# Optimization experiments

Measured on AMD Instinct MI355X. Metric: run time of the kernel, lower is better.

The kernel has to match this reference:

```python
import jax, jax.numpy as jnp
import numpy as np

D_MODEL = 1024
N_SH = 16            # sub-heads per branch
N_BR = 4             # branches
H_TOT = N_BR * N_SH  # 64 total heads
DH = D_MODEL // N_SH # 64 head dim
BRANCH_CONFIGS = [(16, 0), (128, 16), (128, 0), (512, 144)]


def rms_norm(x):
    eps = jnp.finfo(x.dtype).eps
    return x * jax.lax.rsqrt(jnp.mean(x * x, axis=-1, keepdims=True) + eps)


def rope(x):
    # x: [B, H, T, Dh]; non-standard RoPE: even/odd split, halves concatenated
    T, Dh = x.shape[2], x.shape[3]
    inv_freq = 1.0 / (10000.0 ** (jnp.arange(0, Dh, 2, dtype=jnp.float32) / Dh))
    freqs = jnp.arange(T, dtype=jnp.float32)[:, None] * inv_freq[None, :]  # [T, Dh/2]
    cos = jnp.cos(freqs)[None, None]
    sin = jnp.sin(freqs)[None, None]
    x1 = x[..., 0::2]
    x2 = x[..., 1::2]
    return jnp.concatenate([-x2 * sin + x1 * cos, x1 * sin + x2 * cos], axis=-1)


def setup_inputs() -> dict:
    key = jax.random.key(0)
    ks = jax.random.split(key, 12)
    B, T, C = 2, 1024, D_MODEL
    s = 0.02
    return {
        "X": jax.random.normal(ks[0], (B, T, C), jnp.float32),
        "WQ": jax.random.normal(ks[1], (C, H_TOT * DH), jnp.float32) * s,
        "bQ": jax.random.normal(ks[2], (H_TOT * DH,), jnp.float32) * s,
        "WK": jax.random.normal(ks[3], (C, C), jnp.float32) * s,
        "bK": jax.random.normal(ks[4], (C,), jnp.float32) * s,
        "WV": jax.random.normal(ks[5], (C, H_TOT * DH), jnp.float32) * s,
        "bV": jax.random.normal(ks[6], (H_TOT * DH,), jnp.float32) * s,
        "WO": jax.random.normal(ks[7], (C, C), jnp.float32) * s,
        "bO": jax.random.normal(ks[8], (C,), jnp.float32) * s,
        "sink_scalars": jax.random.normal(ks[9], (H_TOT,), jnp.float32) * s,
        "v_nulls": jax.random.normal(ks[10], (H_TOT, DH), jnp.float32) * s,
    }


def reference(X, WQ, bQ, WK, bK, WV, bV, WO, bO, sink_scalars, v_nulls):
    B, T, C = X.shape
    # projections -> [B, H, T, Dh]
    q = (X @ WQ + bQ).reshape(B, T, H_TOT, DH).transpose(0, 2, 1, 3)
    q = rope(rms_norm(q))
    v = (X @ WV + bV).reshape(B, T, H_TOT, DH).transpose(0, 2, 1, 3)
    k = rope((X @ WK + bK).reshape(B, T, N_SH, DH).transpose(0, 2, 1, 3))
    k = jnp.tile(k, (1, N_BR, 1, 1))  # [B, H_TOT, T, Dh]

    # KMax scores with key self-norm denominator
    scores = jnp.einsum('bhqd,bhkd->bhqk', q, k)
    denom = jnp.sqrt(jnp.sum(k * k, axis=-1))[:, :, None, :]  # [B,H,1,T]
    w = scores / denom

    # banded masks per branch; note: off-band logits become 0 (NOT -inf) -> exp(0)=1 in softmax
    idx = jnp.arange(T)
    dist = idx[:, None] - idx[None, :]  # query - key
    bmasks = jnp.stack([((dist >= g) & (dist < h)).astype(w.dtype)
                        for (h, g) in BRANCH_CONFIGS], axis=0)  # [N_BR,T,T]
    full_mask = jnp.repeat(bmasks, N_SH, axis=0)[None]  # [1,H_TOT,T,T] (band subset of tril)
    w = w * full_mask

    # learnable tanh sink logit per head, concatenated as extra column
    sinks = jnp.broadcast_to(jnp.tanh(sink_scalars).reshape(1, H_TOT, 1, 1), (B, H_TOT, T, 1))
    probs = jax.nn.softmax(jnp.concatenate([w, sinks], axis=-1), axis=-1)

    out = jnp.einsum('bhqk,bhkd->bhqd', probs[..., :T], v)
    out = out + probs[..., T:] * v_nulls.reshape(1, H_TOT, 1, DH)

    # [B,H_TOT,T,Dh] -> [B,N_BR,T,C]
    ctx = out.reshape(B, N_BR, N_SH, T, DH).transpose(0, 1, 3, 2, 4).reshape(B, N_BR, T, C)
    y = ctx @ WO + bO
    return y.mean(axis=1)
```

## Files before the change

kernel.cpp:

```cpp
#include <hip/hip_runtime.h>
#include <hip/hip_bf16.h>
#include <math.h>

#define T_SEQ 1024
#define LOG2_10000 13.287712379549449f

typedef unsigned short u16;
typedef unsigned int u32;
typedef __attribute__((ext_vector_type(8))) short bf16x8;
typedef __attribute__((ext_vector_type(4))) float f32x4;

__device__ __forceinline__ void gload16(const u16* g, const u16* s) {
  __builtin_amdgcn_global_load_lds(
      (const __attribute__((address_space(1))) void*)g,
      (__attribute__((address_space(3))) void*)s, 16, 0, 0);
}

__device__ __forceinline__ u16 f2bf(float x) {
  __hip_bfloat16 h = __float2bfloat16(x);
  return *reinterpret_cast<u16*>(&h);
}
__device__ __forceinline__ float bf2f(u16 x) {
  __hip_bfloat16 h = *reinterpret_cast<__hip_bfloat16*>(&x);
  return __bfloat162float(h);
}

__device__ __forceinline__ void transpose_step(
    const float* __restrict__ W, u16* __restrict__ Wt, int N, int nbx,
    int local, int t, float (*tile)[33]) {
  int bx = local % nbx, by = local / nbx;
  int n0 = bx * 32, k0 = by * 32;
  int r = t >> 3, c4 = (t & 7) * 4;
  float4 v = *reinterpret_cast<const float4*>(&W[(size_t)(k0 + r) * N + n0 + c4]);
  tile[r][c4 + 0] = v.x;
  tile[r][c4 + 1] = v.y;
  tile[r][c4 + 2] = v.z;
  tile[r][c4 + 3] = v.w;
  __syncthreads();
  u16 o[4];
#pragma unroll
  for (int i = 0; i < 4; ++i) o[i] = f2bf(tile[c4 + i][r]);
  *reinterpret_cast<uint2*>(&Wt[(size_t)(n0 + r) * 1024 + k0 + c4]) =
      *reinterpret_cast<const uint2*>(o);
}

__global__ __launch_bounds__(256) void prep_kernel(
    const float* __restrict__ X, const float* __restrict__ WQ,
    const float* __restrict__ WK, const float* __restrict__ WV,
    const float* __restrict__ WO, const float* __restrict__ bQ,
    const float* __restrict__ bV, const float* __restrict__ bK,
    u16* __restrict__ Xb, u16* __restrict__ WQVKt, u16* __restrict__ WOt,
    float* __restrict__ bQVK, float* __restrict__ ctab, float* __restrict__ stab)
{
  __shared__ float tile[32][33];
  const int blk = blockIdx.x, t = threadIdx.x;
  if (blk < 128) {
    int id = blk * 256 + t;
    int tt = id >> 5, p = id & 31;
    float invf = exp2f(-LOG2_10000 * (float)(2 * p) * (1.0f / 64.0f));
    float ang = (float)tt * invf;
    float sn, cs;
    sincosf(ang, &sn, &cs);
    ctab[id] = cs;
    stab[id] = sn;
  } else if (blk < 1152) {
    int i = (blk - 128) * 256 + t;
    float4 a = reinterpret_cast<const float4*>(X)[2 * i];
    float4 b = reinterpret_cast<const float4*>(X)[2 * i + 1];
    u16 o[8] = {f2bf(a.x), f2bf(a.y), f2bf(a.z), f2bf(a.w),
                f2bf(b.x), f2bf(b.y), f2bf(b.z), f2bf(b.w)};
    reinterpret_cast<uint4*>(Xb)[i] = *reinterpret_cast<const uint4*>(o);
  } else if (blk < 5248) {
    transpose_step(WQ, WQVKt, 4096, 128, blk - 1152, t, tile);
  } else if (blk < 9344) {
    transpose_step(WV, WQVKt + (size_t)4096 * 1024, 4096, 128, blk - 5248, t, tile);
  } else if (blk < 10368) {
    transpose_step(WK, WQVKt + (size_t)8192 * 1024, 1024, 32, blk - 9344, t, tile);
  } else if (blk < 11392) {
    transpose_step(WO, WOt, 1024, 32, blk - 10368, t, tile);
  } else {
    int id = (blk - 11392) * 256 + t;
    if (id < 9216)
      bQVK[id] = (id < 4096) ? bQ[id] : (id < 8192) ? bV[id - 4096] : bK[id - 8192];
  }
}

__global__ __launch_bounds__(256) void xsum_part_kernel(
    const float* __restrict__ X, float* __restrict__ part) {
  int blk = blockIdx.x;
  int b = blk >> 6, tc = blk & 63;
  const float* base = X + (size_t)(b * 1024 + tc * 16) * 1024;
  for (int kk = threadIdx.x; kk < 1024; kk += 256) {
    float s = 0.f;
#pragma unroll
    for (int tt = 0; tt < 16; ++tt) s += base[(size_t)tt * 1024 + kk];
    part[(size_t)blk * 1024 + kk] = s;
  }
}

__global__ __launch_bounds__(256) void xsum_reduce_kernel(
    const float* __restrict__ part, float* __restrict__ Xsum) {
  int id = blockIdx.x * 256 + threadIdx.x;
  int b = id >> 10, k = id & 1023;
  float s = 0.f;
#pragma unroll 8
  for (int i = 0; i < 64; ++i) s += part[(size_t)(b * 64 + i) * 1024 + k];
  Xsum[id] = s;
}

__global__ __launch_bounds__(256) void vgemv_part_kernel(
    const float* __restrict__ Xsum, const float* __restrict__ WV,
    float* __restrict__ part2) {
  __shared__ float xs0[128], xs1[128];
  int blk = blockIdx.x;
  int nc = blk & 15, ks = blk >> 4;
  int n = nc * 256 + threadIdx.x;
  int k0 = ks * 128;
  if (threadIdx.x < 128) xs0[threadIdx.x] = Xsum[k0 + threadIdx.x];
  else xs1[threadIdx.x - 128] = Xsum[1024 + k0 + threadIdx.x - 128];
  __syncthreads();
  float a0 = 0.f, a1 = 0.f;
  for (int k = 0; k < 128; ++k) {
    float w = WV[(size_t)(k0 + k) * 4096 + n];
    a0 = fmaf(xs0[k], w, a0);
    a1 = fmaf(xs1[k], w, a1);
  }
  part2[(size_t)(ks * 2 + 0) * 4096 + n] = a0;
  part2[(size_t)(ks * 2 + 1) * 4096 + n] = a1;
}

__global__ __launch_bounds__(256) void vgemv_reduce_kernel(
    const float* __restrict__ part2, const float* __restrict__ bV,
    float* __restrict__ Vsum) {
  int id = blockIdx.x * 256 + threadIdx.x;
  int b = id >> 12, n = id & 4095;
  float s = 1024.0f * bV[n];
#pragma unroll
  for (int ks = 0; ks < 8; ++ks) s += part2[(size_t)(ks * 2 + b) * 4096 + n];
  Vsum[id] = s;
}

__global__ __launch_bounds__(512, 1) void gemm8ph_kernel(
    const u16* __restrict__ Ab, const u16* __restrict__ Bt,
    const float* __restrict__ bias, u16* __restrict__ Cqv)
{
  __shared__ __align__(16) u16 sAb[2][256 * 64];
  __shared__ __align__(16) u16 sBb[2][256 * 64];

  const int tid = threadIdx.x;
  const int lane = tid & 63;
  const int w = tid >> 6;
  const int wm = w >> 2, wn = w & 3;
  const int l15 = lane & 15, l4 = lane >> 4;

  int lin = blockIdx.y * 32 + blockIdx.x;
  lin = (lin & 7) * 32 + (lin >> 3);
  const int bx = lin & 31, by = lin >> 5;
  const int m0 = by * 256, bn0 = bx * 256;

  const int srow = tid >> 3;
  const int csw = (tid & 7) ^ (srow & 7);
  const u16* a_base = Ab + (size_t)(m0 + srow) * 1024 + 8 * csw;
  const u16* b_base = Bt + (size_t)(bn0 + srow) * 1024 + 8 * csw;

  const int ch0 = (0 + l4) ^ (l15 & 7);
  const int ch1 = (4 + l4) ^ (l15 & 7);

  f32x4 acc[8][4];
#pragma unroll
  for (int i = 0; i < 8; ++i)
#pragma unroll
    for (int j = 0; j < 4; ++j) acc[i][j] = (f32x4){0.f, 0.f, 0.f, 0.f};

#define STAGE8(kt, buf)                                                        \
  {                                                                            \
    const u16* ga = a_base + (kt) * 64;                                        \
    const u16* gb = b_base + (kt) * 64;                                        \
    u16* da = &sAb[buf][tid * 8];                                              \
    u16* db = &sBb[buf][tid * 8];                                              \
    _Pragma("unroll") for (int q = 0; q < 4; ++q) {                            \
      gload16(ga + q * 65536, da + q * 4096);                                  \
      gload16(gb + q * 65536, db + q * 4096);                                  \
    }                                                                          \
  }

  STAGE8(0, 0);
#pragma unroll 1
  for (int kt = 0; kt < 16; ++kt) {
    const int buf = kt & 1;
    if (kt < 15) {
      STAGE8(kt + 1, buf ^ 1);
      asm volatile("s_waitcnt vmcnt(8)" ::: "memory");
    } else {
      asm volatile("s_waitcnt vmcnt(0)" ::: "memory");
    }
    __builtin_amdgcn_sched_barrier(0);
    __builtin_amdgcn_s_barrier();
    __builtin_amdgcn_sched_barrier(0);

    const u16* tA = sAb[buf];
    const u16* tB = sBb[buf];

    bf16x8 bfv[4][2];
#pragma unroll
    for (int n = 0; n < 4; ++n) {
      int row = wn * 64 + n * 16 + l15;
      bfv[n][0] = *reinterpret_cast<const bf16x8*>(&tB[row * 64 + ch0 * 8]);
      bfv[n][1] = *reinterpret_cast<const bf16x8*>(&tB[row * 64 + ch1 * 8]);
    }
#pragma unroll
    for (int mh = 0; mh < 2; ++mh) {
      bf16x8 af[4][2];
#pragma unroll
      for (int m = 0; m < 4; ++m) {
        int row = wm * 128 + mh * 64 + m * 16 + l15;
        af[m][0] = *reinterpret_cast<const bf16x8*>(&tA[row * 64 + ch0 * 8]);
        af[m][1] = *reinterpret_cast<const bf16x8*>(&tA[row * 64 + ch1 * 8]);
      }
      __builtin_amdgcn_s_setprio(1);
#pragma unroll
      for (int kk = 0; kk < 2; ++kk)
#pragma unroll
        for (int m = 0; m < 4; ++m)
#pragma unroll
          for (int n = 0; n < 4; ++n)
            acc[mh * 4 + m][n] = __builtin_amdgcn_mfma_f32_16x16x32_bf16(
                af[m][kk], bfv[n][kk], acc[mh * 4 + m][n], 0, 0, 0);
      __builtin_amdgcn_s_setprio(0);
    }
    __builtin_amdgcn_s_barrier();
    __builtin_amdgcn_sched_barrier(0);
  }
#undef STAGE8

#pragma unroll
  for (int n = 0; n < 4; ++n) {
    int col = bn0 + wn * 64 + n * 16 + l15;
    float bv = bias[col];
#pragma unroll
    for (int mf = 0; mf < 8; ++mf) {
#pragma unroll
      for (int r = 0; r < 4; ++r) {
        int row = m0 + wm * 128 + mf * 16 + l4 * 4 + r;
        Cqv[(size_t)row * 8192 + col] = f2bf(acc[mf][n][r] + bv);
      }
    }
  }
}

template <bool BF16OUT>
__global__ __launch_bounds__(256) void gemm64_kernel(
    const u16* __restrict__ Ab, const u16* __restrict__ Bt,
    const float* __restrict__ bias, void* __restrict__ Cv,
    int M, int N, int K)
{
  __shared__ __align__(16) u16 sA[64 * 32];
  __shared__ __align__(16) u16 sB[64 * 32];
  const int tid = threadIdx.x;
  const int lane = tid & 63;
  const int wv = tid >> 6;
  const int wm = wv >> 1, wn = wv & 1;
  const int l15 = lane & 15, l4 = lane >> 4;
  const int m0 = blockIdx.y * 64, n0 = blockIdx.x * 64;

  f32x4 acc[2][2];
#pragma unroll
  for (int i = 0; i < 2; ++i)
#pragma unroll
    for (int j = 0; j < 2; ++j) acc[i][j] = (f32x4){0.f, 0.f, 0.f, 0.f};

  const int r0 = tid >> 2, kc = tid & 3;
  const u16* a_src = Ab + (size_t)(m0 + r0) * K + kc * 8;
  const u16* b_src = Bt + (size_t)(n0 + r0) * K + kc * 8;
  u16* dA = sA + (size_t)wv * 512;
  u16* dB = sB + (size_t)wv * 512;
  const int kcol = l4 * 8;

  for (int k0 = 0; k0 < K; k0 += 32) {
    __syncthreads();
    gload16(a_src + k0, dA);
    gload16(b_src + k0, dB);
    __syncthreads();
    bf16x8 af[2], bfv[2];
#pragma unroll
    for (int mi = 0; mi < 2; ++mi)
      af[mi] = *reinterpret_cast<const bf16x8*>(&sA[(wm * 32 + mi * 16 + l15) * 32 + kcol]);
#pragma unroll
    for (int ni = 0; ni < 2; ++ni)
      bfv[ni] = *reinterpret_cast<const bf16x8*>(&sB[(wn * 32 + ni * 16 + l15) * 32 + kcol]);
#pragma unroll
    for (int mi = 0; mi < 2; ++mi)
#pragma unroll
      for (int ni = 0; ni < 2; ++ni)
        acc[mi][ni] = __builtin_amdgcn_mfma_f32_16x16x32_bf16(
            af[mi], bfv[ni], acc[mi][ni], 0, 0, 0);
  }

#pragma unroll
  for (int mi = 0; mi < 2; ++mi)
#pragma unroll
    for (int ni = 0; ni < 2; ++ni) {
      int col = n0 + wn * 32 + ni * 16 + l15;
      float bv = bias[col];
#pragma unroll
      for (int r = 0; r < 4; ++r) {
        int row = m0 + wm * 32 + mi * 16 + l4 * 4 + r;
        float val = acc[mi][ni][r] + bv;
        size_t idx = (size_t)row * N + col;
        if (BF16OUT) ((u16*)Cv)[idx] = f2bf(val);
        else ((float*)Cv)[idx] = val;
      }
    }
}

__global__ __launch_bounds__(256) void qk_transform_kernel(
    u16* __restrict__ QVbf, u16* __restrict__ Kbf,
    const float* __restrict__ ctab, const float* __restrict__ stab)
{
  const int rid  = blockIdx.x * 8 + (threadIdx.x >> 5);
  const int lane = threadIdx.x & 63;
  const int p    = lane & 31;
  const int gb   = lane & 32;

  u16* row;
  int t;
  const bool isQ = rid < 131072;
  if (isQ) {
    int h = rid & 63, bt = rid >> 6;
    t = bt & 1023;
    row = QVbf + (size_t)bt * 8192 + h * 64;
  } else {
    int r2 = rid - 131072;
    int hsL = r2 & 15, bt = r2 >> 4;
    t = bt & 1023;
    row = Kbf + (size_t)bt * 1024 + hsL * 64;
  }

  u32 v = reinterpret_cast<const u32*>(row)[p];
  float x1 = bf2f((u16)v), x2 = bf2f((u16)(v >> 16));
  float cs = ctab[t * 32 + p], sn = stab[t * 32 + p];

  float o_lo, o_hi;
  if (isQ) {
    float ss = x1 * x1 + x2 * x2;
    ss += __shfl_xor(ss, 1, 64);
    ss += __shfl_xor(ss, 2, 64);
    ss += __shfl_xor(ss, 4, 64);
    ss += __shfl_xor(ss, 8, 64);
    ss += __shfl_xor(ss, 16, 64);
    float rs = rsqrtf(ss * (1.0f / 64.0f) + 1.1920929e-7f);
    float xn1 = x1 * rs, xn2 = x2 * rs;
    o_lo = xn1 * cs - xn2 * sn;
    o_hi = xn1 * sn + xn2 * cs;
  } else {
    float xr1 = x1 * cs - x2 * sn;
    float xr2 = x1 * sn + x2 * cs;
    float ss = xr1 * xr1 + xr2 * xr2;
    ss += __shfl_xor(ss, 1, 64);
    ss += __shfl_xor(ss, 2, 64);
    ss += __shfl_xor(ss, 4, 64);
    ss += __shfl_xor(ss, 8, 64);
    ss += __shfl_xor(ss, 16, 64);
    float rs = rsqrtf(ss);
    o_lo = xr1 * rs;
    o_hi = xr2 * rs;
  }

  int m = (2 * p) & 31;
  float slo0 = __shfl(o_lo, gb + m, 64);
  float slo1 = __shfl(o_lo, gb + m + 1, 64);
  float shi0 = __shfl(o_hi, gb + m, 64);
  float shi1 = __shfl(o_hi, gb + m + 1, 64);
  float e0 = (p < 16) ? slo0 : shi0;
  float e1 = (p < 16) ? slo1 : shi1;
  reinterpret_cast<u32*>(row)[p] = (u32)f2bf(e0) | ((u32)f2bf(e1) << 16);
}

__global__ __launch_bounds__(256) void attn_mfma_kernel(
    const u16* __restrict__ Qv, const u16* __restrict__ Kb,
    const float* __restrict__ Vsum, const float* __restrict__ sink,
    const float* __restrict__ vnull, u16* __restrict__ mctxb)
{
  __shared__ __align__(16) u16 sQ[64 * 64];
  __shared__ __align__(16) u16 sK[2][64 * 64];
  __shared__ __align__(16) u16 sVt[2][64 * 64];
  __shared__ __align__(16) u16 sP[64 * 64];

  int blk = blockIdx.x;
  blk = (blk & 7) * 64 + (blk >> 3);
  const int qt  = blk & 15;
  const int hs  = (blk >> 4) & 15;
  const int b   = blk >> 8;
  const int qt0 = qt * 64;

  const int tid  = threadIdx.x;
  const int lane = tid & 63;
  const int wv   = tid >> 6;
  const int l15  = lane & 15;
  const int l4   = lane >> 4;
  const int qr0  = tid >> 3, qi0 = tid & 7;
  const int qr1  = qr0 + 32;
  const int vjp  = tid & 31, vdg = tid >> 5;
  const int qrow = wv * 16 + l15;

  constexpr int HCFG[4] = {16, 128, 128, 512};
  constexpr int GCFG[4] = {0, 16, 0, 144};

  f32x4 macc[4];
#pragma unroll
  for (int i = 0; i < 4; ++i) macc[i] = (f32x4){0.f, 0.f, 0.f, 0.f};

#pragma unroll 1
  for (int br = 0; br < 4; ++br) {
    const int h = br * 16 + hs;
    const int hmax = HCFG[br], g = GCFG[br];
    int klo = qt0 - (hmax - 1); if (klo < 0) klo = 0;
    int khi = qt0 + 63 - g;     if (khi > 1023) khi = 1023;
    const int nc = (khi >= klo) ? ((khi - klo) / 64 + 1) : 0;

    gload16(Qv + (size_t)(b * 1024 + qt0 + qr0) * 8192 + h * 64 + 8 * (qi0 ^ (qr0 & 7)),
            sQ + (size_t)wv * 512);
    gload16(Qv + (size_t)(b * 1024 + qt0 + qr1) * 8192 + h * 64 + 8 * (qi0 ^ (qr1 & 7)),
            sQ + 2048 + (size_t)wv * 512);
    bf16x8 va, vb;
    if (nc > 0) {
      int ja0 = klo + qr0; if (ja0 > 1023) ja0 = 1023;
      int ja1 = klo + qr1; if (ja1 > 1023) ja1 = 1023;
      gload16(Kb + (size_t)(b * 1024 + ja0) * 1024 + hs * 64 + 8 * (qi0 ^ (qr0 & 7)),
              sK[0] + (size_t)wv * 512);
      gload16(Kb + (size_t)(b * 1024 + ja1) * 1024 + hs * 64 + 8 * (qi0 ^ (qr1 & 7)),
              sK[0] + 2048 + (size_t)wv * 512);
      int jva = klo + 2 * vjp, jvb = jva + 1;
      if (jva > 1023) jva = 1023;
      if (jvb > 1023) jvb = 1023;
      va = *reinterpret_cast<const bf16x8*>(
          &Qv[(size_t)(b * 1024 + jva) * 8192 + 4096 + h * 64 + vdg * 8]);
      vb = *reinterpret_cast<const bf16x8*>(
          &Qv[(size_t)(b * 1024 + jvb) * 8192 + 4096 + h * 64 + vdg * 8]);
    }
    asm volatile("s_waitcnt vmcnt(0)" ::: "memory");
    __builtin_amdgcn_sched_barrier(0);
    if (nc > 0) {
#pragma unroll
      for (int e = 0; e < 8; ++e) {
        int d = vdg * 8 + e;
        u32 pack = (u32)(u16)va[e] | ((u32)(u16)vb[e] << 16);
        *reinterpret_cast<u32*>(
            (char*)sVt[0] + d * 128 + ((4 * vjp) ^ ((d & 7) << 4))) = pack;
      }
    }
    asm volatile("s_waitcnt lgkmcnt(0)" ::: "memory");
    __builtin_amdgcn_sched_barrier(0);
    __builtin_amdgcn_s_barrier();

    bf16x8 afQ[2];
#pragma unroll
    for (int kh = 0; kh < 2; ++kh) {
      int cs = (4 * kh + l4) ^ (l15 & 7);
      afQ[kh] = *reinterpret_cast<const bf16x8*>(&sQ[qrow * 64 + cs * 8]);
    }

    f32x4 outv[4];
#pragma unroll
    for (int i = 0; i < 4; ++i) outv[i] = (f32x4){0.f, 0.f, 0.f, 0.f};
    float zacc[4] = {0.f, 0.f, 0.f, 0.f};

    int buf = 0;
#pragma unroll 1
    for (int c = 0; c < nc; ++c) {
      const int j0 = klo + c * 64;
      const bool nxt = (c + 1 < nc);
      if (nxt) {
        int j0n = j0 + 64;
        int ja0 = j0n + qr0; if (ja0 > 1023) ja0 = 1023;
        int ja1 = j0n + qr1; if (ja1 > 1023) ja1 = 1023;
        gload16(Kb + (size_t)(b * 1024 + ja0) * 1024 + hs * 64 + 8 * (qi0 ^ (qr0 & 7)),
                sK[buf ^ 1] + (size_t)wv * 512);
        gload16(Kb + (size_t)(b * 1024 + ja1) * 1024 + hs * 64 + 8 * (qi0 ^ (qr1 & 7)),
                sK[buf ^ 1] + 2048 + (size_t)wv * 512);
        int jva = j0n + 2 * vjp, jvb = jva + 1;
        if (jva > 1023) jva = 1023;
        if (jvb > 1023) jvb = 1023;
        va = *reinterpret_cast<const bf16x8*>(
            &Qv[(size_t)(b * 1024 + jva) * 8192 + 4096 + h * 64 + vdg * 8]);
        vb = *reinterpret_cast<const bf16x8*>(
            &Qv[(size_t)(b * 1024 + jvb) * 8192 + 4096 + h * 64 + vdg * 8]);
      }
      f32x4 sfr[4];
#pragma unroll
      for (int jt = 0; jt < 4; ++jt) {
        int krow = jt * 16 + l15;
        f32x4 acc = (f32x4){0.f, 0.f, 0.f, 0.f};
#pragma unroll
        for (int kh = 0; kh < 2; ++kh) {
          int cs = (4 * kh + l4) ^ (l15 & 7);
          bf16x8 bk = *reinterpret_cast<const bf16x8*>(&sK[buf][krow * 64 + cs * 8]);
          acc = __builtin_amdgcn_mfma_f32_16x16x32_bf16(afQ[kh], bk, acc, 0, 0, 0);
        }
        sfr[jt] = acc;
      }
#pragma unroll
      for (int jt = 0; jt < 4; ++jt) {
        int jloc = jt * 16 + l15;
        int jabs = j0 + jloc;
#pragma unroll
        for (int r = 0; r < 4; ++r) {
          int q_r = wv * 16 + l4 * 4 + r;
          int dist = (qt0 + q_r) - jabs;
          bool inband = (dist >= g) & (dist < hmax) & (jabs < 1024);
          float pv = inband ? (__expf(sfr[jt][r]) - 1.0f) : 0.0f;
          zacc[r] += pv;
          *reinterpret_cast<u16*>(
              (char*)sP + q_r * 128 + ((2 * jloc) ^ ((q_r & 7) << 4))) = f2bf(pv);
        }
      }
      asm volatile("s_waitcnt lgkmcnt(0)" ::: "memory");
      __builtin_amdgcn_sched_barrier(0);
      bf16x8 afP[2];
#pragma unroll
      for (int kh = 0; kh < 2; ++kh) {
        int cs = (4 * kh + l4) ^ (l15 & 7);
        afP[kh] = *reinterpret_cast<const bf16x8*>(&sP[qrow * 64 + cs * 8]);
      }
#pragma unroll
      for (int dt = 0; dt < 4; ++dt) {
        int drow = dt * 16 + l15;
#pragma unroll
        for (int kh = 0; kh < 2; ++kh) {
          int cs = (4 * kh + l4) ^ (l15 & 7);
          bf16x8 bv = *reinterpret_cast<const bf16x8*>(&sVt[buf][drow * 64 + cs * 8]);
          outv[dt] = __builtin_amdgcn_mfma_f32_16x16x32_bf16(afP[kh], bv, outv[dt], 0, 0, 0);
        }
      }
      if (nxt) {
#pragma unroll
        for (int e = 0; e < 8; ++e) {
          int d = vdg * 8 + e;
          u32 pack = (u32)(u16)va[e] | ((u32)(u16)vb[e] << 16);
          *reinterpret_cast<u32*>(
              (char*)sVt[buf ^ 1] + d * 128 + ((4 * vjp) ^ ((d & 7) << 4))) = pack;
        }
      }
      asm volatile("s_waitcnt vmcnt(0) lgkmcnt(0)" ::: "memory");
      __builtin_amdgcn_sched_barrier(0);
      __builtin_amdgcn_s_barrier();
      buf ^= 1;
    }

#pragma unroll
    for (int r = 0; r < 4; ++r) {
      zacc[r] += __shfl_xor(zacc[r], 1, 64);
      zacc[r] += __shfl_xor(zacc[r], 2, 64);
      zacc[r] += __shfl_xor(zacc[r], 4, 64);
      zacc[r] += __shfl_xor(zacc[r], 8, 64);
    }
    float es = __expf(tanhf(sink[h]));
#pragma unroll
    for (int dt = 0; dt < 4; ++dt) {
      int d = dt * 16 + l15;
      float vs = Vsum[(size_t)b * 4096 + h * 64 + d];
      float vn = vnull[h * 64 + d];
#pragma unroll
      for (int r = 0; r < 4; ++r) {
        float invZ = 1.0f / (1024.0f + zacc[r] + es);
        macc[dt][r] += (outv[dt][r] + vs + es * vn) * invZ;
      }
    }
  }

#pragma unroll
  for (int dt = 0; dt < 4; ++dt) {
#pragma unroll
    for (int r = 0; r < 4; ++r) {
      int q_r = wv * 16 + l4 * 4 + r;
      mctxb[(size_t)(b * 1024 + qt0 + q_r) * 1024 + hs * 64 + dt * 16 + l15] =
          f2bf(0.25f * macc[dt][r]);
    }
  }
}

extern "C" void kernel_launch(void* const* d_in, const int* in_sizes, int n_in,
                              void* d_out, int out_size, void* d_ws, size_t ws_size,
                              hipStream_t stream) {
  (void)in_sizes; (void)n_in; (void)out_size; (void)ws_size;
  const float* X    = (const float*)d_in[0];
  const float* WQ   = (const float*)d_in[1];
  const float* bQ   = (const float*)d_in[2];
  const float* WK   = (const float*)d_in[3];
  const float* bK   = (const float*)d_in[4];
  const float* WV   = (const float*)d_in[5];
  const float* bV   = (const float*)d_in[6];
  const float* WO   = (const float*)d_in[7];
  const float* bO   = (const float*)d_in[8];
  const float* sink = (const float*)d_in[9];
  const float* vnul = (const float*)d_in[10];
  float* Y = (float*)d_out;

  char* p = (char*)d_ws;
  u16*   Xb    = (u16*)p;   p += (size_t)2048 * 1024 * 2;
  u16*   WQVKt = (u16*)p;   p += (size_t)9216 * 1024 * 2;
  u16*   WOt   = (u16*)p;   p += (size_t)1024 * 1024 * 2;
  u16*   QVbf  = (u16*)p;   p += (size_t)2048 * 8192 * 2;
  u16*   Kbf   = (u16*)p;   p += (size_t)2048 * 1024 * 2;
  u16*   mctxb = (u16*)p;   p += (size_t)2048 * 1024 * 2;
  float* Vsum  = (float*)p; p += (size_t)2 * 4096 * 4;
  float* part  = (float*)p; p += (size_t)128 * 1024 * 4;
  float* Xsum  = (float*)p; p += (size_t)2 * 1024 * 4;
  float* part2 = (float*)p; p += (size_t)16 * 4096 * 4;
  float* bQVK  = (float*)p; p += (size_t)9216 * 4;
  float* ctab  = (float*)p; p += (size_t)32768 * 4;
  float* stab  = (float*)p; p += (size_t)32768 * 4;

  dim3 blk(256);
  prep_kernel<<<11428, blk, 0, stream>>>(X, WQ, WK, WV, WO, bQ, bV, bK,
                                         Xb, WQVKt, WOt, bQVK, ctab, stab);
  xsum_part_kernel<<<128, blk, 0, stream>>>(X, part);
  xsum_reduce_kernel<<<8, blk, 0, stream>>>(part, Xsum);
  vgemv_part_kernel<<<128, blk, 0, stream>>>(Xsum, WV, part2);
  vgemv_reduce_kernel<<<32, blk, 0, stream>>>(part2, bV, Vsum);

  gemm8ph_kernel<<<dim3(32, 8), dim3(512), 0, stream>>>(Xb, WQVKt, bQVK, QVbf);
  gemm64_kernel<true><<<dim3(16, 32), blk, 0, stream>>>(
      Xb, WQVKt + (size_t)8192 * 1024, bQVK + 8192, Kbf, 2048, 1024, 1024);

  qk_transform_kernel<<<20480, blk, 0, stream>>>(QVbf, Kbf, ctab, stab);

  attn_mfma_kernel<<<512, blk, 0, stream>>>(QVbf, Kbf, Vsum, sink, vnul, mctxb);

  gemm64_kernel<false><<<dim3(16, 32), blk, 0, stream>>>(mctxb, WOt, bO, Y, 2048, 1024, 1024);
}
```

Baseline: 151.6 us.

## Restructure QV GEMM pipeline and compute V column sums from projected V

The QV projection GEMM switches from a 2-stage pipeline with K-tile 64 to a 4-slot ring with K-tile 32 and prefetch depth 2. It also drops the trailing per-iteration barrier and remaps blocks to XCDs with a new LDS swizzle. The V column-sum path no longer sums X and runs a GEMV with fp32 WV. Instead it sums the bf16 V outputs already produced by the GEMM, which cuts two kernels and the fp32 WV read but adds bf16 rounding to Vsum. Removing the trailing barrier relies on the 4-slot ring to avoid overwriting a buffer that is still being read.

Result: faster. 139.7 us (-7.9%).

```diff
diff --git a/kernel.cpp b/kernel.cpp
--- a/kernel.cpp
+++ b/kernel.cpp
@@ -23,6 +23,16 @@
 __device__ __forceinline__ float bf2f(u16 x) {
   __hip_bfloat16 h = *reinterpret_cast<__hip_bfloat16*>(&x);
   return __bfloat162float(h);
+}
+
+__device__ __forceinline__ float wave_sum64(float v) {
+  v += __shfl_xor(v, 1, 64);
+  v += __shfl_xor(v, 2, 64);
+  v += __shfl_xor(v, 4, 64);
+  v += __shfl_xor(v, 8, 64);
+  v += __shfl_xor(v, 16, 64);
+  v += __shfl_xor(v, 32, 64);
+  return v;
 }
 
 __device__ __forceinline__ void transpose_step(
@@ -85,67 +95,43 @@
   }
 }
 
-__global__ __launch_bounds__(256) void xsum_part_kernel(
-    const float* __restrict__ X, float* __restrict__ part) {
+__global__ __launch_bounds__(256) void vsum_part_kernel(
+    const u16* __restrict__ QVbf, float* __restrict__ part) {
   int blk = blockIdx.x;
-  int b = blk >> 6, tc = blk & 63;
-  const float* base = X + (size_t)(b * 1024 + tc * 16) * 1024;
-  for (int kk = threadIdx.x; kk < 1024; kk += 256) {
-    float s = 0.f;
-#pragma unroll
-    for (int tt = 0; tt < 16; ++tt) s += base[(size_t)tt * 1024 + kk];
-    part[(size_t)blk * 1024 + kk] = s;
-  }
-}
-
-__global__ __launch_bounds__(256) void xsum_reduce_kernel(
-    const float* __restrict__ part, float* __restrict__ Xsum) {
+  int b = blk >> 6, ch = blk & 63;
+  const u16* base = QVbf + (size_t)(b * 1024 + ch * 16) * 8192 + 4096;
+#pragma unroll
+  for (int g = 0; g < 2; ++g) {
+    int c0 = (threadIdx.x + g * 256) * 8;
+    float s[8] = {0.f, 0.f, 0.f, 0.f, 0.f, 0.f, 0.f, 0.f};
+#pragma unroll 4
+    for (int r = 0; r < 16; ++r) {
+      bf16x8 v = *reinterpret_cast<const bf16x8*>(&base[(size_t)r * 8192 + c0]);
+#pragma unroll
+      for (int e = 0; e < 8; ++e) s[e] += bf2f((u16)v[e]);
+    }
+    float* dst = &part[(size_t)blk * 4096 + c0];
+#pragma unroll
+    for (int e = 0; e < 8; ++e) dst[e] = s[e];
+  }
+}
+
+__global__ __launch_bounds__(256) void vsum_reduce_kernel(
+    const float* __restrict__ part, float* __restrict__ Vsum) {
   int id = blockIdx.x * 256 + threadIdx.x;
-  int b = id >> 10, k = id & 1023;
+  int b = id >> 12, n = id & 4095;
   float s = 0.f;
 #pragma unroll 8
-  for (int i = 0; i < 64; ++i) s += part[(size_t)(b * 64 + i) * 1024 + k];
-  Xsum[id] = s;
-}
-
-__global__ __launch_bounds__(256) void vgemv_part_kernel(
-    const float* __restrict__ Xsum, const float* __restrict__ WV,
-    float* __restrict__ part2) {
-  __shared__ float xs0[128], xs1[128];
-  int blk = blockIdx.x;
-  int nc = blk & 15, ks = blk >> 4;
-  int n = nc * 256 + threadIdx.x;
-  int k0 = ks * 128;
-  if (threadIdx.x < 128) xs0[threadIdx.x] = Xsum[k0 + threadIdx.x];
-  else xs1[threadIdx.x - 128] = Xsum[1024 + k0 + threadIdx.x - 128];
-  __syncthreads();
-  float a0 = 0.f, a1 = 0.f;
-  for (int k = 0; k < 128; ++k) {
-    float w = WV[(size_t)(k0 + k) * 4096 + n];
-    a0 = fmaf(xs0[k], w, a0);
-    a1 = fmaf(xs1[k], w, a1);
-  }
-  part2[(size_t)(ks * 2 + 0) * 4096 + n] = a0;
-  part2[(size_t)(ks * 2 + 1) * 4096 + n] = a1;
-}
-
-__global__ __launch_bounds__(256) void vgemv_reduce_kernel(
-    const float* __restrict__ part2, const float* __restrict__ bV,
-    float* __restrict__ Vsum) {
-  int id = blockIdx.x * 256 + threadIdx.x;
-  int b = id >> 12, n = id & 4095;
-  float s = 1024.0f * bV[n];
-#pragma unroll
-  for (int ks = 0; ks < 8; ++ks) s += part2[(size_t)(ks * 2 + b) * 4096 + n];
+  for (int ch = 0; ch < 64; ++ch) s += part[(size_t)(b * 64 + ch) * 4096 + n];
   Vsum[id] = s;
 }
 
-__global__ __launch_bounds__(512, 1) void gemm8ph_kernel(
+__global__ __launch_bounds__(512, 1) void gemm_qv_kernel(
     const u16* __restrict__ Ab, const u16* __restrict__ Bt,
     const float* __restrict__ bias, u16* __restrict__ Cqv)
 {
-  __shared__ __align__(16) u16 sAb[2][256 * 64];
-  __shared__ __align__(16) u16 sBb[2][256 * 64];
+  __shared__ __align__(16) u16 sA[4][256 * 32];
+  __shared__ __align__(16) u16 sB[4][256 * 32];
 
   const int tid = threadIdx.x;
   const int lane = tid & 63;
@@ -153,44 +139,48 @@
   const int wm = w >> 2, wn = w & 3;
   const int l15 = lane & 15, l4 = lane >> 4;
 
-  int lin = blockIdx.y * 32 + blockIdx.x;
-  lin = (lin & 7) * 32 + (lin >> 3);
-  const int bx = lin & 31, by = lin >> 5;
-  const int m0 = by * 256, bn0 = bx * 256;
-
-  const int srow = tid >> 3;
-  const int csw = (tid & 7) ^ (srow & 7);
-  const u16* a_base = Ab + (size_t)(m0 + srow) * 1024 + 8 * csw;
-  const u16* b_base = Bt + (size_t)(bn0 + srow) * 1024 + 8 * csw;
-
-  const int ch0 = (0 + l4) ^ (l15 & 7);
-  const int ch1 = (4 + l4) ^ (l15 & 7);
+  const int orig = blockIdx.x;
+  const int xcd = orig & 7, j = orig >> 3;
+  const int by = (xcd >> 2) * 4 + (j >> 3);
+  const int bx = (xcd & 3) * 8 + (j & 7);
+  const int m0 = by * 256, n0 = bx * 256;
+
+  const int r0s = tid >> 2,         c0s = tid & 3;
+  const int r1s = (512 + tid) >> 2, c1s = (512 + tid) & 3;
+  const int sc0 = c0s ^ ((r0s >> 1) & 3);
+  const int sc1 = c1s ^ ((r1s >> 1) & 3);
+  const u16* aA0 = Ab + (size_t)(m0 + r0s) * 1024 + 8 * sc0;
+  const u16* aA1 = Ab + (size_t)(m0 + r1s) * 1024 + 8 * sc1;
+  const u16* aB0 = Bt + (size_t)(n0 + r0s) * 1024 + 8 * sc0;
+  const u16* aB1 = Bt + (size_t)(n0 + r1s) * 1024 + 8 * sc1;
+
+  const int cp = l4 ^ ((l15 >> 1) & 3);
 
   f32x4 acc[8][4];
 #pragma unroll
   for (int i = 0; i < 8; ++i)
 #pragma unroll
-    for (int j = 0; j < 4; ++j) acc[i][j] = (f32x4){0.f, 0.f, 0.f, 0.f};
-
-#define STAGE8(kt, buf)                                                        \
+    for (int jn = 0; jn < 4; ++jn) acc[i][jn] = (f32x4){0.f, 0.f, 0.f, 0.f};
+
+#define STAGE32(t)                                                             \
   {                                                                            \
-    const u16* ga = a_base + (kt) * 64;                                        \
-    const u16* gb = b_base + (kt) * 64;                                        \
-    u16* da = &sAb[buf][tid * 8];                                              \
-    u16* db = &sBb[buf][tid * 8];                                              \
-    _Pragma("unroll") for (int q = 0; q < 4; ++q) {                            \
-      gload16(ga + q * 65536, da + q * 4096);                                  \
-      gload16(gb + q * 65536, db + q * 4096);                                  \
-    }                                                                          \
-  }
-
-  STAGE8(0, 0);
+    const int sl = (t) & 3;                                                    \
+    const int ko = (t) * 32;                                                   \
+    gload16(aA0 + ko, &sA[sl][tid * 8]);                                       \
+    gload16(aA1 + ko, &sA[sl][4096 + tid * 8]);                                \
+    gload16(aB0 + ko, &sB[sl][tid * 8]);                                       \
+    gload16(aB1 + ko, &sB[sl][4096 + tid * 8]);                                \
+  }
+
+  STAGE32(0);
+  STAGE32(1);
 #pragma unroll 1
-  for (int kt = 0; kt < 16; ++kt) {
-    const int buf = kt & 1;
-    if (kt < 15) {
-      STAGE8(kt + 1, buf ^ 1);
+  for (int t = 0; t < 32; ++t) {
+    if (t + 2 < 32) {
+      STAGE32(t + 2);
       asm volatile("s_waitcnt vmcnt(8)" ::: "memory");
+    } else if (t + 1 < 32) {
+      asm volatile("s_waitcnt vmcnt(4)" ::: "memory");
     } else {
       asm volatile("s_waitcnt vmcnt(0)" ::: "memory");
     }
@@ -198,44 +188,35 @@
     __builtin_amdgcn_s_barrier();
     __builtin_amdgcn_sched_barrier(0);
 
-    const u16* tA = sAb[buf];
-    const u16* tB = sBb[buf];
-
-    bf16x8 bfv[4][2];
+    const u16* tA = sA[t & 3];
+    const u16* tB = sB[t & 3];
+
+    bf16x8 bf[4];
 #pragma unroll
     for (int n = 0; n < 4; ++n) {
       int row = wn * 64 + n * 16 + l15;
-      bfv[n][0] = *reinterpret_cast<const bf16x8*>(&tB[row * 64 + ch0 * 8]);
-      bfv[n][1] = *reinterpret_cast<const bf16x8*>(&tB[row * 64 + ch1 * 8]);
-    }
-#pragma unroll
-    for (int mh = 0; mh < 2; ++mh) {
-      bf16x8 af[4][2];
-#pragma unroll
-      for (int m = 0; m < 4; ++m) {
-        int row = wm * 128 + mh * 64 + m * 16 + l15;
-        af[m][0] = *reinterpret_cast<const bf16x8*>(&tA[row * 64 + ch0 * 8]);
-        af[m][1] = *reinterpret_cast<const bf16x8*>(&tA[row * 64 + ch1 * 8]);
-      }
-      __builtin_amdgcn_s_setprio(1);
-#pragma unroll
-      for (int kk = 0; kk < 2; ++kk)
-#pragma unroll
-        for (int m = 0; m < 4; ++m)
-#pragma unroll
-          for (int n = 0; n < 4; ++n)
-            acc[mh * 4 + m][n] = __builtin_amdgcn_mfma_f32_16x16x32_bf16(
-                af[m][kk], bfv[n][kk], acc[mh * 4 + m][n], 0, 0, 0);
-      __builtin_amdgcn_s_setprio(0);
-    }
-    __builtin_amdgcn_s_barrier();
-    __builtin_amdgcn_sched_barrier(0);
-  }
-#undef STAGE8
+      bf[n] = *reinterpret_cast<const bf16x8*>(&tB[row * 32 + cp * 8]);
+    }
+    bf16x8 af[8];
+#pragma unroll
+    for (int m = 0; m < 8; ++m) {
+      int row = wm * 128 + m * 16 + l15;
+      af[m] = *reinterpret_cast<const bf16x8*>(&tA[row * 32 + cp * 8]);
+    }
+    __builtin_amdgcn_s_setprio(1);
+#pragma unroll
+    for (int m = 0; m < 8; ++m)
+#pragma unroll
+      for (int n = 0; n < 4; ++n)
+        acc[m][n] = __builtin_amdgcn_mfma_f32_16x16x32_bf16(
+            af[m], bf[n], acc[m][n], 0, 0, 0);
+    __builtin_amdgcn_s_setprio(0);
+  }
+#undef STAGE32
 
 #pragma unroll
   for (int n = 0; n < 4; ++n) {
-    int col = bn0 + wn * 64 + n * 16 + l15;
+    int col = n0 + wn * 64 + n * 16 + l15;
     float bv = bias[col];
 #pragma unroll
     for (int mf = 0; mf < 8; ++mf) {
@@ -604,9 +585,7 @@
   u16*   Kbf   = (u16*)p;   p += (size_t)2048 * 1024 * 2;
   u16*   mctxb = (u16*)p;   p += (size_t)2048 * 1024 * 2;
   float* Vsum  = (float*)p; p += (size_t)2 * 4096 * 4;
-  float* part  = (float*)p; p += (size_t)128 * 1024 * 4;
-  float* Xsum  = (float*)p; p += (size_t)2 * 1024 * 4;
-  float* part2 = (float*)p; p += (size_t)16 * 4096 * 4;
+  float* vpart = (float*)p; p += (size_t)128 * 4096 * 4;
   float* bQVK  = (float*)p; p += (size_t)9216 * 4;
   float* ctab  = (float*)p; p += (size_t)32768 * 4;
   float* stab  = (float*)p; p += (size_t)32768 * 4;
@@ -614,15 +593,14 @@
   dim3 blk(256);
   prep_kernel<<<11428, blk, 0, stream>>>(X, WQ, WK, WV, WO, bQ, bV, bK,
                                          Xb, WQVKt, WOt, bQVK, ctab, stab);
-  xsum_part_kernel<<<128, blk, 0, stream>>>(X, part);
-  xsum_reduce_kernel<<<8, blk, 0, stream>>>(part, Xsum);
-  vgemv_part_kernel<<<128, blk, 0, stream>>>(Xsum, WV, part2);
-  vgemv_reduce_kernel<<<32, blk, 0, stream>>>(part2, bV, Vsum);
-
-  gemm8ph_kernel<<<dim3(32, 8), dim3(512), 0, stream>>>(Xb, WQVKt, bQVK, QVbf);
+
+  gemm_qv_kernel<<<256, dim3(512), 0, stream>>>(Xb, WQVKt, bQVK, QVbf);
   gemm64_kernel<true><<<dim3(16, 32), blk, 0, stream>>>(
       Xb, WQVKt + (size_t)8192 * 1024, bQVK + 8192, Kbf, 2048, 1024, 1024);
 
+  vsum_part_kernel<<<128, blk, 0, stream>>>(QVbf, vpart);
+  vsum_reduce_kernel<<<32, blk, 0, stream>>>(vpart, Vsum);
+
   qk_transform_kernel<<<20480, blk, 0, stream>>>(QVbf, Kbf, ctab, stab);
 
   attn_mfma_kernel<<<512, blk, 0, stream>>>(QVbf, Kbf, Vsum, sink, vnul, mctxb);
```
